# Kernel tuning notes

Hardware: AMD Instinct MI355X
Metric: run time of the kernel (lower is better)

Reference implementation:

```python
import jax, jax.numpy as jnp
import numpy as np

B, L, N = 32, 4096, 256
FFT_K = 5
MAX_FREQ_LEVELS = 4
LAGS = [1, 3, 6, 12, 24]


def setup_inputs() -> dict:
    key = jax.random.key(0)
    k0, k1, k2, k3, k4 = jax.random.split(key, 5)
    x = jax.random.normal(k0, (B, L, N), dtype=jnp.float32)
    # depth_gate: Linear(2->8), GELU, Linear(8->1)  (stored as x @ W + b)
    dg_w1 = jax.random.normal(k1, (2, 8), dtype=jnp.float32) * 0.5
    dg_b1 = jax.random.normal(k2, (8,), dtype=jnp.float32) * 0.1
    dg_w2 = jax.random.normal(k3, (8, 1), dtype=jnp.float32) * 0.3
    dg_b2 = jax.random.normal(k4, (1,), dtype=jnp.float32) * 0.1
    return {"x": x, "dg_w1": dg_w1, "dg_b1": dg_b1, "dg_w2": dg_w2, "dg_b2": dg_b2}


def reference(x, dg_w1, dg_b1, dg_w2, dg_b2):
    eps = 1e-8
    # ---- moment statistics (over time dim=1), torch.std is unbiased (ddof=1) ----
    mean = x.mean(axis=1, keepdims=True)                     # (B,1,N)
    std = jnp.std(x, axis=1, ddof=1, keepdims=True)          # (B,1,N)
    std_e = std + eps
    diff = x - mean
    skew = (diff ** 3).mean(axis=1, keepdims=True) / (std_e ** 3 + eps)
    kurt = (diff ** 4).mean(axis=1, keepdims=True) / (std_e ** 4 + eps) - 3.0

    # ---- FFT features with iterative multi-level top-k extraction ----
    amp = jnp.abs(jnp.fft.rfft(x, axis=1))                   # (B,F,N)
    F_bins = amp.shape[1]
    freqs = jnp.arange(F_bins, dtype=jnp.float32) / L        # (F,)
    amp_T = jnp.transpose(amp, (0, 2, 1))                    # (B,N,F)

    residual = amp_T
    aggregated = jnp.zeros_like(amp_T)
    total_energy = amp_T.mean(axis=-1, keepdims=True) + eps
    running = jnp.ones((B, N, 1), dtype=x.dtype)
    bidx = jnp.arange(B)[:, None, None]
    nidx = jnp.arange(N)[None, :, None]
    for level in range(MAX_FREQ_LEVELS):
        k_level = min(max(1, int(round(FFT_K / 2 ** level))), F_bins)
        level_amp, level_idx = jax.lax.top_k(residual, k_level)
        level_map = jnp.zeros_like(residual).at[bidx, nidx, level_idx].set(level_amp)
        residual_ratio = residual.mean(axis=-1, keepdims=True) / total_energy
        level_ratio = jnp.full_like(residual_ratio, float(level + 1) / MAX_FREQ_LEVELS)
        gate_in = jnp.concatenate([residual_ratio, level_ratio], axis=-1)    # (B,N,2)
        h = jax.nn.gelu(gate_in @ dg_w1 + dg_b1, approximate=False)
        need_deeper = jax.nn.sigmoid(h @ dg_w2 + dg_b2)                      # (B,N,1)
        aggregated = aggregated + running * level_map
        residual = residual - level_map
        running = running * need_deeper

    # hard top-k decode
    top_amp, top_idx = jax.lax.top_k(aggregated, FFT_K)      # (B,N,k)
    top_freqs = freqs[top_idx]                               # (B,N,k)
    max_amp = amp_T.max(axis=-1, keepdims=True) + eps
    top_amp_norm = top_amp / (max_amp + eps)
    fft_feat = jnp.concatenate([top_freqs, top_amp_norm], axis=-1)   # (B,N,2k)
    fft_feat = jnp.transpose(fft_feat, (0, 2, 1))                    # (B,2k,N)

    # ---- autocorrelation at fixed lags ----
    x_norm = diff / std_e
    ac = jnp.stack(
        [(x_norm[:, :-lag, :] * x_norm[:, lag:, :]).mean(axis=1) for lag in LAGS],
        axis=1,
    )  # (B, n_lags, N)

    feats = jnp.concatenate([mean, std, skew, kurt, fft_feat, ac], axis=1)  # (B,19,N)
    return jnp.transpose(feats, (0, 2, 1))  # (B,N,19)
```

## Files before the change

kernel.cpp:

```cpp
#include <hip/hip_runtime.h>
#include <math.h>

#define B_    32
#define L_    4096
#define N_    256
#define NC    2048
#define NSEG  32
#define SEGLEN (L_ / NSEG)
#define CHUNK 32
#define NCH   (SEGLEN / CHUNK)
#define NQ    9
#define NCAND 8

__device__ __forceinline__ int PD(int i) { return i + (i >> 3); }

__global__ __launch_bounds__(256, 4) void k_stats_trans(const float* __restrict__ x,
                                                        float* __restrict__ P,
                                                        float* __restrict__ xt,
                                                        int do_t) {
  __shared__ float tile[CHUNK][N_ + 1];
  const int s = blockIdx.x;
  const int b = blockIdx.y;
  const int n = threadIdx.x;
  const int l0 = s * SEGLEN;
  const float* xp = x + (size_t)b * L_ * N_ + n;
  float* xtb = xt + (size_t)b * N_ * L_;

  float prev[CHUNK];
#pragma unroll
  for (int j = 0; j < CHUNK; ++j) {
    const int l = l0 - CHUNK + j;
    prev[j] = (l >= 0) ? xp[(size_t)l * N_] : 0.0f;
  }
  float s1 = 0.f, s2 = 0.f, s3 = 0.f, s4 = 0.f;
  float c1 = 0.f, c3 = 0.f, c6 = 0.f, c12 = 0.f, c24 = 0.f;
  for (int c = 0; c < NCH; ++c) {
    const int lb = l0 + c * CHUNK;
    float cur[CHUNK];
#pragma unroll
    for (int j = 0; j < CHUNK; ++j) cur[j] = xp[(size_t)(lb + j) * N_];
#pragma unroll
    for (int j = 0; j < CHUNK; ++j) {
      const float v = cur[j], v2 = v * v;
      s1 += v; s2 += v2; s3 += v2 * v; s4 += v2 * v2;
    }
#pragma unroll
    for (int j = 0; j < CHUNK; ++j) {
      const float v = cur[j];
      c1  += v * ((j >= 1)  ? cur[j - 1]  : prev[CHUNK + j - 1]);
      c3  += v * ((j >= 3)  ? cur[j - 3]  : prev[CHUNK + j - 3]);
      c6  += v * ((j >= 6)  ? cur[j - 6]  : prev[CHUNK + j - 6]);
      c12 += v * ((j >= 12) ? cur[j - 12] : prev[CHUNK + j - 12]);
      c24 += v * ((j >= 24) ? cur[j - 24] : prev[CHUNK + j - 24]);
    }
    if (do_t) {
#pragma unroll
      for (int j = 0; j < CHUNK; ++j) tile[j][n] = cur[j];
      __syncthreads();
#pragma unroll
      for (int it = 0; it < 8; ++it) {
        const int g  = n + 256 * it;
        const int np = g >> 3;
        const int j4 = g & 7;
        float4 w;
        w.x = tile[4 * j4 + 0][np];
        w.y = tile[4 * j4 + 1][np];
        w.z = tile[4 * j4 + 2][np];
        w.w = tile[4 * j4 + 3][np];
        *(float4*)(xtb + (size_t)np * L_ + lb + 4 * j4) = w;
      }
      __syncthreads();
    }
#pragma unroll
    for (int j = 0; j < CHUNK; ++j) prev[j] = cur[j];
  }
  float* Pp = P + (size_t)(s * B_ + b) * NQ * N_ + n;
  Pp[0 * N_] = s1; Pp[1 * N_] = s2; Pp[2 * N_] = s3; Pp[3 * N_] = s4;
  Pp[4 * N_] = c1; Pp[5 * N_] = c3; Pp[6 * N_] = c6; Pp[7 * N_] = c12; Pp[8 * N_] = c24;
}

__global__ __launch_bounds__(256) void k_stats_final(const float* __restrict__ x,
                                                     const float* __restrict__ P,
                                                     float* __restrict__ out) {
  const int b = blockIdx.x;
  const int n = threadIdx.x;
  float S[NQ];
#pragma unroll
  for (int q = 0; q < NQ; ++q) S[q] = 0.0f;
  for (int s = 0; s < NSEG; ++s) {
    const float* Pp = P + (size_t)(s * B_ + b) * NQ * N_ + n;
#pragma unroll
    for (int q = 0; q < NQ; ++q) S[q] += Pp[q * N_];
  }
  const float Lf = (float)L_;
  const float mu = S[0] / Lf;
  float ssd = S[1] - Lf * mu * mu;
  ssd = fmaxf(ssd, 0.0f);
  const float stdv = sqrtf(ssd / (Lf - 1.0f));
  const float se  = stdv + 1e-8f;
  const float m3 = (S[2] - 3.0f * mu * S[1] + 2.0f * Lf * mu * mu * mu) / Lf;
  const float m4 = (S[3] - 4.0f * mu * S[2] + 6.0f * mu * mu * S[1]
                    - 3.0f * Lf * mu * mu * mu * mu) / Lf;
  const float se2 = se * se;
  const float skew = m3 / (se2 * se + 1e-8f);
  const float kurt = m4 / (se2 * se2 + 1e-8f) - 3.0f;

  const float* xp = x + (size_t)b * L_ * N_ + n;
  float hl[5], tl[5];
  {
    float hs = 0.0f, ts = 0.0f;
#pragma unroll
    for (int t = 0; t < 24; ++t) {
      hs += xp[(size_t)t * N_];
      ts += xp[(size_t)(L_ - 1 - t) * N_];
      if (t == 0)  { hl[0] = hs; tl[0] = ts; }
      if (t == 2)  { hl[1] = hs; tl[1] = ts; }
      if (t == 5)  { hl[2] = hs; tl[2] = ts; }
      if (t == 11) { hl[3] = hs; tl[3] = ts; }
      if (t == 23) { hl[4] = hs; tl[4] = ts; }
    }
  }
  float* op = out + ((size_t)b * N_ + n) * 19;
  op[0] = mu; op[1] = stdv; op[2] = skew; op[3] = kurt;
  const int lags[5] = {1, 3, 6, 12, 24};
  const float inv_se2 = 1.0f / se2;
#pragma unroll
  for (int i = 0; i < 5; ++i) {
    const float cnt = (float)(L_ - lags[i]);
    const float SA = S[0] - tl[i];
    const float SB = S[0] - hl[i];
    const float num = S[4 + i] - mu * (SA + SB) + cnt * mu * mu;
    op[14 + i] = num * inv_se2 / cnt;
  }
}

__device__ __forceinline__ void dft8(float (&vr)[8], float (&vi)[8]) {
  const float C7 = 0.70710678118654752f;
  float t0r = vr[0] + vr[4], t0i = vi[0] + vi[4];
  float t1r = vr[0] - vr[4], t1i = vi[0] - vi[4];
  float t2r = vr[2] + vr[6], t2i = vi[2] + vi[6];
  float t3r = vr[2] - vr[6], t3i = vi[2] - vi[6];
  float E0r = t0r + t2r, E0i = t0i + t2i;
  float E2r = t0r - t2r, E2i = t0i - t2i;
  float E1r = t1r + t3i, E1i = t1i - t3r;
  float E3r = t1r - t3i, E3i = t1i + t3r;
  float u0r = vr[1] + vr[5], u0i = vi[1] + vi[5];
  float u1r = vr[1] - vr[5], u1i = vi[1] - vi[5];
  float u2r = vr[3] + vr[7], u2i = vi[3] + vi[7];
  float u3r = vr[3] - vr[7], u3i = vi[3] - vi[7];
  float O0r = u0r + u2r, O0i = u0i + u2i;
  float O2r = u0r - u2r, O2i = u0i - u2i;
  float O1r = u1r + u3i, O1i = u1i - u3r;
  float O3r = u1r - u3i, O3i = u1i + u3r;
  vr[0] = E0r + O0r; vi[0] = E0i + O0i;
  vr[4] = E0r - O0r; vi[4] = E0i - O0i;
  float a1r = C7 * (O1r + O1i), a1i = C7 * (O1i - O1r);
  vr[1] = E1r + a1r; vi[1] = E1i + a1i;
  vr[5] = E1r - a1r; vi[5] = E1i - a1i;
  vr[2] = E2r + O2i; vi[2] = E2i - O2r;
  vr[6] = E2r - O2i; vi[6] = E2i + O2r;
  float a3r = C7 * (O3i - O3r), a3i = -C7 * (O3r + O3i);
  vr[3] = E3r + a3r; vi[3] = E3i + a3i;
  vr[7] = E3r - a3r; vi[7] = E3i - a3i;
}

__device__ __forceinline__ void twid8(float (&vr)[8], float (&vi)[8], float w1r, float w1i) {
  float w2r = w1r * w1r - w1i * w1i, w2i = 2.f * w1r * w1i;
  float w3r = w2r * w1r - w2i * w1i, w3i = w2r * w1i + w2i * w1r;
  float w4r = w2r * w2r - w2i * w2i, w4i = 2.f * w2r * w2i;
  float w5r = w3r * w2r - w3i * w2i, w5i = w3r * w2i + w3i * w2r;
  float w6r = w3r * w3r - w3i * w3i, w6i = 2.f * w3r * w3i;
  float w7r = w4r * w3r - w4i * w3i, w7i = w4r * w3i + w4i * w3r;
  float t;
  t = vr[1] * w1r - vi[1] * w1i; vi[1] = vr[1] * w1i + vi[1] * w1r; vr[1] = t;
  t = vr[2] * w2r - vi[2] * w2i; vi[2] = vr[2] * w2i + vi[2] * w2r; vr[2] = t;
  t = vr[3] * w3r - vi[3] * w3i; vi[3] = vr[3] * w3i + vi[3] * w3r; vr[3] = t;
  t = vr[4] * w4r - vi[4] * w4i; vi[4] = vr[4] * w4i + vi[4] * w4r; vr[4] = t;
  t = vr[5] * w5r - vi[5] * w5i; vi[5] = vr[5] * w5i + vi[5] * w5r; vr[5] = t;
  t = vr[6] * w6r - vi[6] * w6i; vi[6] = vr[6] * w6i + vi[6] * w6r; vr[6] = t;
  t = vr[7] * w7r - vi[7] * w7i; vi[7] = vr[7] * w7i + vi[7] * w7r; vr[7] = t;
}

__global__ __launch_bounds__(256, 4) void k_fft_top(const float* __restrict__ base, int stride,
                                                    float* __restrict__ out) {
  __shared__ float XR[2304];
  __shared__ float XI[2304];
  __shared__ float TWR[256];
  __shared__ float TWI[256];
  __shared__ float RV[4];
  __shared__ int   RI[4];
  __shared__ float TOPV[NCAND];
  __shared__ int   TOPI[NCAND];
  __shared__ double DA[NCAND];
  __shared__ int REFINE;
  const int tid = threadIdx.x;
  const int bn  = blockIdx.x;

  const float ang = -3.14159265358979323846f * (float)tid * (1.0f / 2048.0f);
  const float s4 = __sinf(ang), c4 = __cosf(ang);
  const float tb4r = c4, tb4i = s4;
  const float cn = c4 * c4 - s4 * s4;
  const float sn = 2.0f * c4 * s4;
  TWR[tid] = cn; TWI[tid] = sn;

  float vr[8], vi[8];
  if (stride == 1) {
    const float2* src2 = (const float2*)(base + (size_t)bn * L_);
#pragma unroll
    for (int r = 0; r < 8; ++r) {
      const float2 v = src2[tid + 256 * r];
      vr[r] = v.x; vi[r] = v.y;
    }
  } else {
    const float* src = base + (size_t)(bn >> 8) * ((size_t)L_ * N_) + (bn & (N_ - 1));
#pragma unroll
    for (int r = 0; r < 8; ++r) {
      vr[r] = src[(size_t)(2 * (tid + 256 * r)) * N_];
      vi[r] = src[(size_t)(2 * (tid + 256 * r) + 1) * N_];
    }
  }

  dft8(vr, vi);
  twid8(vr, vi, cn, sn);
#pragma unroll
  for (int m = 0; m < 8; ++m) {
    XR[PD(8 * tid + m)] = vr[m];
    XI[PD(8 * tid + m)] = vi[m];
  }
  __syncthreads();

#pragma unroll
  for (int st = 0; st < 2; ++st) {
    const int s = (st == 0) ? 8 : 64;
#pragma unroll
    for (int r = 0; r < 8; ++r) {
      vr[r] = XR[PD(tid + 256 * r)];
      vi[r] = XI[PD(tid + 256 * r)];
    }
    __syncthreads();
    const int tb = tid & ~(s - 1);
    dft8(vr, vi);
    twid8(vr, vi, TWR[tb], TWI[tb]);
    const int wb = tid + 7 * tb;
#pragma unroll
    for (int m = 0; m < 8; ++m) {
      XR[PD(wb + m * s)] = vr[m];
      XI[PD(wb + m * s)] = vi[m];
    }
    __syncthreads();
  }

  {
    float ar[8], ai[8];
#pragma unroll
    for (int h = 0; h < 2; ++h) {
      const int i = tid + 256 * h;
#pragma unroll
      for (int r = 0; r < 4; ++r) {
        ar[4 * h + r] = XR[PD(i + 512 * r)];
        ai[4 * h + r] = XI[PD(i + 512 * r)];
      }
    }
    __syncthreads();
#pragma unroll
    for (int h = 0; h < 2; ++h) {
      const int i = tid + 256 * h;
      const float x0r = ar[4*h+0], x0i = ai[4*h+0], x1r = ar[4*h+1], x1i = ai[4*h+1];
      const float x2r = ar[4*h+2], x2i = ai[4*h+2], x3r = ar[4*h+3], x3i = ai[4*h+3];
      const float t0r = x0r + x2r, t0i = x0i + x2i;
      const float t1r = x0r - x2r, t1i = x0i - x2i;
      const float t2r = x1r + x3r, t2i = x1i + x3i;
      const float t3r = x1r - x3r, t3i = x1i - x3i;
      XR[PD(i)]        = t0r + t2r;  XI[PD(i)]        = t0i + t2i;
      XR[PD(i + 512)]  = t1r + t3i;  XI[PD(i + 512)]  = t1i - t3r;
      XR[PD(i + 1024)] = t0r - t2r;  XI[PD(i + 1024)] = t0i - t2i;
      XR[PD(i + 1536)] = t1r - t3i;  XI[PD(i + 1536)] = t1i + t3r;
    }
    __syncthreads();
  }

  const float WAC[4] = {1.f, 0.92387953f, 0.70710678f, 0.38268343f};
  const float WAS[4] = {0.f, 0.38268343f, 0.70710678f, 0.92387953f};
  float av[4], am[4];
#pragma unroll
  for (int j = 0; j < 4; ++j) {
    const int k  = tid + 256 * j;
    const int kr = (2048 - k) & 2047;
    const float zar = XR[PD(k)],  zai = XI[PD(k)];
    const float zbr = XR[PD(kr)], zbi = -XI[PD(kr)];
    const float Er = 0.5f * (zar + zbr), Ei = 0.5f * (zai + zbi);
    const float Or = 0.5f * (zai - zbi), Oi = -0.5f * (zar - zbr);
    const float cv = WAC[j] * tb4r + WAS[j] * tb4i;
    const float sv = WAC[j] * tb4i - WAS[j] * tb4r;
    const float pr = cv * Or - sv * Oi, pi = cv * Oi + sv * Or;
    const float Xr = Er + pr, Xi = Ei + pi;
    const float Mr = Er - pr, Mi = Ei - pi;
    av[j] = sqrtf(Xr * Xr + Xi * Xi);
    am[j] = sqrtf(Mr * Mr + Mi * Mi);
  }
  float a1024 = -1.f;
  if (tid == 0) {
    const float zr = XR[PD(1024)], zi = XI[PD(1024)];
    a1024 = sqrtf(zr * zr + zi * zi);
  }
  __syncthreads();
  float* amp = XR;
#pragma unroll
  for (int j = 0; j < 4; ++j) {
    amp[tid + 256 * j] = av[j];
    amp[2048 - tid - 256 * j] = am[j];
  }
  if (tid == 0) amp[1024] = a1024;
  __syncthreads();

  const int lane = tid & 63, wid = tid >> 6;
  float bv = -1.f; int bi = 1 << 30;
#pragma unroll
  for (int j = 0; j < 4; ++j) {
    const int k = tid + 256 * j;
    if (av[j] > bv || (av[j] == bv && k < bi)) { bv = av[j]; bi = k; }
    const int mk = 2048 - k;
    if (am[j] > bv || (am[j] == bv && mk < bi)) { bv = am[j]; bi = mk; }
  }
  if (tid == 0 && (a1024 > bv || (a1024 == bv && 1024 < bi))) { bv = a1024; bi = 1024; }

  for (int rr = 0; rr < NCAND; ++rr) {
    float rv = bv; int ri = bi;
#pragma unroll
    for (int off = 32; off > 0; off >>= 1) {
      const float v2 = __shfl_down(rv, off);
      const int   i2 = __shfl_down(ri, off);
      if (v2 > rv || (v2 == rv && i2 < ri)) { rv = v2; ri = i2; }
    }
    if (lane == 0) { RV[wid] = rv; RI[wid] = ri; }
    __syncthreads();
    if (tid == 0) {
      float mv = RV[0]; int mi = RI[0];
#pragma unroll
      for (int w = 1; w < 4; ++w) {
        if (RV[w] > mv || (RV[w] == mv && RI[w] < mi)) { mv = RV[w]; mi = RI[w]; }
      }
      TOPV[rr] = mv; TOPI[rr] = mi;
      amp[mi] = -1.f;
    }
    __syncthreads();
    const int w = TOPI[rr];
    if (((w & 255) == tid) || (((2048 - w) & 255) == tid)) {
      bv = -1.f; bi = 1 << 30;
#pragma unroll
      for (int j = 0; j < 4; ++j) {
        const int k = tid + 256 * j;
        const float v = amp[k];
        if (v > bv || (v == bv && k < bi)) { bv = v; bi = k; }
        const int mk = 2048 - k;
        const float v2 = amp[mk];
        if (v2 > bv || (v2 == bv && mk < bi)) { bv = v2; bi = mk; }
      }
      if (tid == 0) {
        const float v = amp[1024];
        if (v > bv || (v == bv && 1024 < bi)) { bv = v; bi = 1024; }
      }
    }
  }

  if (tid == 0) {
    int need = 0;
    const float thr = 1e-3f * TOPV[0];
#pragma unroll
    for (int r = 0; r < 5; ++r) {
      if (TOPV[r] - TOPV[r + 1] < thr) need = 1;
    }
    REFINE = need;
  }
  __syncthreads();

  if (REFINE) {
    const int g = tid >> 5;
    const int j = tid & 31;
    const int k = TOPI[g];
    const int t0 = 128 * j;
    const int e0 = (int)(((long long)k * (long long)t0) & 4095LL);
    double sp, cp;  sincos(-2.0 * 3.14159265358979323846 * (double)e0 / 4096.0, &sp, &cp);
    double sw, cw;  sincos(-2.0 * 3.14159265358979323846 * (double)k  / 4096.0, &sw, &cw);
    double ar = 0.0, ai = 0.0;
    if (stride == 1) {
      const float* xr_ = base + (size_t)bn * L_ + t0;
      for (int t = 0; t < 128; ++t) {
        const double xv = (double)xr_[t];
        ar += xv * cp; ai += xv * sp;
        const double ncp = cp * cw - sp * sw;
        sp = cp * sw + sp * cw; cp = ncp;
      }
    } else {
      const float* xr_ = base + (size_t)(bn >> 8) * ((size_t)L_ * N_) + (bn & (N_ - 1));
      for (int t = 0; t < 128; ++t) {
        const double xv = (double)xr_[(size_t)(t0 + t) * N_];
        ar += xv * cp; ai += xv * sp;
        const double ncp = cp * cw - sp * sw;
        sp = cp * sw + sp * cw; cp = ncp;
      }
    }
#pragma unroll
    for (int off = 16; off > 0; off >>= 1) {
      ar += __shfl_down(ar, off, 32);
      ai += __shfl_down(ai, off, 32);
    }
    if (j == 0) DA[g] = sqrt(ar * ar + ai * ai);
    __syncthreads();
    if (tid == 0) {
      double da[NCAND]; int di[NCAND];
#pragma unroll
      for (int r = 0; r < NCAND; ++r) { da[r] = DA[r]; di[r] = TOPI[r]; }
      for (int i2 = 1; i2 < NCAND; ++i2) {
        const double v = da[i2]; const int ii = di[i2];
        int p = i2 - 1;
        while (p >= 0 && (da[p] < v || (da[p] == v && di[p] > ii))) {
          da[p + 1] = da[p]; di[p + 1] = di[p]; --p;
        }
        da[p + 1] = v; di[p + 1] = ii;
      }
      float* op = out + (size_t)bn * 19;
      const double den = da[0] + 2e-8;
#pragma unroll
      for (int r = 0; r < 5; ++r) {
        op[4 + r] = (float)di[r] * (1.0f / (float)L_);
        op[9 + r] = (float)(da[r] / den);
      }
    }
  } else if (tid == 0) {
    float* op = out + (size_t)bn * 19;
    const float den = TOPV[0] + 2e-8f;
#pragma unroll
    for (int r = 0; r < 5; ++r) {
      op[4 + r] = (float)TOPI[r] * (1.0f / (float)L_);
      op[9 + r] = TOPV[r] / den;
    }
  }
}

extern "C" void kernel_launch(void* const* d_in, const int* in_sizes, int n_in,
                              void* d_out, int out_size, void* d_ws, size_t ws_size,
                              hipStream_t stream) {
  const float* x = (const float*)d_in[0];
  float* out = (float*)d_out;
  float* ws  = (float*)d_ws;

  const size_t xt_elems   = (size_t)B_ * N_ * L_;
  const size_t part_elems = (size_t)NSEG * B_ * NQ * N_;
  const bool use_xt = ws_size >= (xt_elems + part_elems) * sizeof(float);
  float* xt = ws;
  float* P  = use_xt ? (ws + xt_elems) : ws;

  k_stats_trans<<<dim3(NSEG, B_), 256, 0, stream>>>(x, P, use_xt ? xt : nullptr,
                                                    use_xt ? 1 : 0);
  k_stats_final<<<B_, 256, 0, stream>>>(x, P, out);
  if (use_xt) {
    k_fft_top<<<B_ * N_, 256, 0, stream>>>(xt, 1, out);
  } else {
    k_fft_top<<<B_ * N_, 256, 0, stream>>>(x, N_, out);
  }
}
```

Before: 358.9 us.

## Keep top-k candidates in registers with double-buffered reductions, fewer barriers

The iterative top-8 selection in the FFT kernel no longer writes amplitudes back to shared memory or relies on thread 0 to pick the winner. Each thread masks its own winning bin in registers and rescans. Every thread redundantly combines the per-wave results from a double-buffered shared array, so each round needs one barrier instead of two, and the refine decision no longer needs a barrier either. Launch bounds go from 4 to 6 blocks per SM. The cost is higher register pressure from keeping the top values in per-thread arrays, which may spill under the tighter launch bound.

After: 365.5 us. About the same (+1.8%).

```diff
diff --git a/kernel.cpp b/kernel.cpp
--- a/kernel.cpp
+++ b/kernel.cpp
@@ -181,18 +181,15 @@
   t = vr[7] * w7r - vi[7] * w7i; vi[7] = vr[7] * w7i + vi[7] * w7r; vr[7] = t;
 }
 
-__global__ __launch_bounds__(256, 4) void k_fft_top(const float* __restrict__ base, int stride,
+__global__ __launch_bounds__(256, 6) void k_fft_top(const float* __restrict__ base, int stride,
                                                     float* __restrict__ out) {
   __shared__ float XR[2304];
   __shared__ float XI[2304];
   __shared__ float TWR[256];
   __shared__ float TWI[256];
-  __shared__ float RV[4];
-  __shared__ int   RI[4];
-  __shared__ float TOPV[NCAND];
-  __shared__ int   TOPI[NCAND];
+  __shared__ float RVb[2][4];
+  __shared__ int   RIb[2][4];
   __shared__ double DA[NCAND];
-  __shared__ int REFINE;
   const int tid = threadIdx.x;
   const int bn  = blockIdx.x;
 
@@ -303,15 +300,6 @@
     const float zr = XR[PD(1024)], zi = XI[PD(1024)];
     a1024 = sqrtf(zr * zr + zi * zi);
   }
-  __syncthreads();
-  float* amp = XR;
-#pragma unroll
-  for (int j = 0; j < 4; ++j) {
-    amp[tid + 256 * j] = av[j];
-    amp[2048 - tid - 256 * j] = am[j];
-  }
-  if (tid == 0) amp[1024] = a1024;
-  __syncthreads();
 
   const int lane = tid & 63, wid = tid >> 6;
   float bv = -1.f; int bi = 1 << 30;
@@ -322,8 +310,10 @@
     const int mk = 2048 - k;
     if (am[j] > bv || (am[j] == bv && mk < bi)) { bv = am[j]; bi = mk; }
   }
-  if (tid == 0 && (a1024 > bv || (a1024 == bv && 1024 < bi))) { bv = a1024; bi = 1024; }
-
+  if (tid == 0 && a1024 > bv) { bv = a1024; bi = 1024; }
+
+  float tv[NCAND]; int ti[NCAND];
+#pragma unroll
   for (int rr = 0; rr < NCAND; ++rr) {
     float rv = bv; int ri = bi;
 #pragma unroll
@@ -332,52 +322,47 @@
       const int   i2 = __shfl_down(ri, off);
       if (v2 > rv || (v2 == rv && i2 < ri)) { rv = v2; ri = i2; }
     }
-    if (lane == 0) { RV[wid] = rv; RI[wid] = ri; }
-    __syncthreads();
-    if (tid == 0) {
-      float mv = RV[0]; int mi = RI[0];
-#pragma unroll
-      for (int w = 1; w < 4; ++w) {
-        if (RV[w] > mv || (RV[w] == mv && RI[w] < mi)) { mv = RV[w]; mi = RI[w]; }
-      }
-      TOPV[rr] = mv; TOPI[rr] = mi;
-      amp[mi] = -1.f;
-    }
-    __syncthreads();
-    const int w = TOPI[rr];
-    if (((w & 255) == tid) || (((2048 - w) & 255) == tid)) {
-      bv = -1.f; bi = 1 << 30;
-#pragma unroll
-      for (int j = 0; j < 4; ++j) {
-        const int k = tid + 256 * j;
-        const float v = amp[k];
-        if (v > bv || (v == bv && k < bi)) { bv = v; bi = k; }
-        const int mk = 2048 - k;
-        const float v2 = amp[mk];
-        if (v2 > bv || (v2 == bv && mk < bi)) { bv = v2; bi = mk; }
-      }
-      if (tid == 0) {
-        const float v = amp[1024];
-        if (v > bv || (v == bv && 1024 < bi)) { bv = v; bi = 1024; }
-      }
-    }
-  }
-
-  if (tid == 0) {
-    int need = 0;
-    const float thr = 1e-3f * TOPV[0];
+    if (lane == 0) { RVb[rr & 1][wid] = rv; RIb[rr & 1][wid] = ri; }
+    __syncthreads();
+    float mv = RVb[rr & 1][0]; int mi = RIb[rr & 1][0];
+#pragma unroll
+    for (int w = 1; w < 4; ++w) {
+      const float v2 = RVb[rr & 1][w]; const int i2 = RIb[rr & 1][w];
+      if (v2 > mv || (v2 == mv && i2 < mi)) { mv = v2; mi = i2; }
+    }
+    tv[rr] = mv; ti[rr] = mi;
+#pragma unroll
+    for (int j = 0; j < 4; ++j) {
+      if (tid + 256 * j == mi) av[j] = -2.f;
+      if (2048 - tid - 256 * j == mi) am[j] = -2.f;
+    }
+    if (tid == 0 && mi == 1024) a1024 = -2.f;
+    bv = -1.f; bi = 1 << 30;
+#pragma unroll
+    for (int j = 0; j < 4; ++j) {
+      const int k = tid + 256 * j;
+      if (av[j] > bv || (av[j] == bv && k < bi)) { bv = av[j]; bi = k; }
+      const int mk = 2048 - k;
+      if (am[j] > bv || (am[j] == bv && mk < bi)) { bv = am[j]; bi = mk; }
+    }
+    if (tid == 0 && a1024 > bv) { bv = a1024; bi = 1024; }
+  }
+
+  int need = 0;
+  {
+    const float thr = 1e-3f * tv[0];
 #pragma unroll
     for (int r = 0; r < 5; ++r) {
-      if (TOPV[r] - TOPV[r + 1] < thr) need = 1;
-    }
-    REFINE = need;
-  }
-  __syncthreads();
-
-  if (REFINE) {
+      if (tv[r] - tv[r + 1] < thr) need = 1;
+    }
+  }
+
+  if (need) {
     const int g = tid >> 5;
     const int j = tid & 31;
-    const int k = TOPI[g];
+    int k = ti[0];
+#pragma unroll
+    for (int r = 1; r < NCAND; ++r) { if (g == r) k = ti[r]; }
     const int t0 = 128 * j;
     const int e0 = (int)(((long long)k * (long long)t0) & 4095LL);
     double sp, cp;  sincos(-2.0 * 3.14159265358979323846 * (double)e0 / 4096.0, &sp, &cp);
@@ -410,7 +395,7 @@
     if (tid == 0) {
       double da[NCAND]; int di[NCAND];
 #pragma unroll
-      for (int r = 0; r < NCAND; ++r) { da[r] = DA[r]; di[r] = TOPI[r]; }
+      for (int r = 0; r < NCAND; ++r) { da[r] = DA[r]; di[r] = ti[r]; }
       for (int i2 = 1; i2 < NCAND; ++i2) {
         const double v = da[i2]; const int ii = di[i2];
         int p = i2 - 1;
@@ -429,11 +414,11 @@
     }
   } else if (tid == 0) {
     float* op = out + (size_t)bn * 19;
-    const float den = TOPV[0] + 2e-8f;
+    const float den = tv[0] + 2e-8f;
 #pragma unroll
     for (int r = 0; r < 5; ++r) {
-      op[4 + r] = (float)TOPI[r] * (1.0f / (float)L_);
-      op[9 + r] = TOPV[r] / den;
+      op[4 + r] = (float)ti[r] * (1.0f / (float)L_);
+      op[9 + r] = tv[r] / den;
     }
   }
 }
```
